# Optimization experiments

Measured on AMD Instinct MI355X. Metric: run time of the kernel, lower is better.

The kernel has to match this reference:

```python
import jax, jax.numpy as jnp
import numpy as np

DT = 0.5  # timestep; CFL-stable for c<1, grid spacing h=1


def laplace5(u):
    # 5-point Laplacian with zero (Dirichlet) boundary, grid spacing 1.
    # u: [B, Nx, Ny]
    z = jnp.pad(u, ((0, 0), (1, 1), (1, 1)))
    return (z[:, 2:, 1:-1] + z[:, :-2, 1:-1]
            + z[:, 1:-1, 2:] + z[:, 1:-1, :-2] - 4.0 * u)


def setup_inputs() -> dict:
    key = jax.random.key(0)
    k1, k2, k3, k4, k5 = jax.random.split(key, 5)
    B, T, Nx, Ny, Np = 16, 256, 256, 256, 3
    x = jax.random.normal(k1, (B, T), dtype=jnp.float32)
    c = jax.random.uniform(k2, (Nx, Ny), dtype=jnp.float32)      # wave speed
    b = jax.random.uniform(k3, (Nx, Ny), dtype=jnp.float32)      # damping (rho)
    px = jax.random.randint(k4, (Np,), 0, Nx)
    py = jax.random.randint(k5, (Np,), 0, Ny)
    return {"x": x, "c": c, "b": b, "px": px, "py": py, "sx": 128, "sy": 128}


def reference(x, c, b, px, py, sx, sy):
    # x: [B, T], c,b: [Nx, Ny]; returns y: [B, T, Np]
    B = x.shape[0]
    Nx, Ny = c.shape
    c1 = 1.0 / (1.0 + 0.5 * DT * b)          # [Nx, Ny]
    c2 = 1.0 - 0.5 * DT * b                  # [Nx, Ny]
    csq_dt2 = (DT * DT) * (c * c)            # [Nx, Ny]
    h0 = jnp.zeros((B, Nx, Ny), dtype=x.dtype)

    def step(carry, xi):
        h1, h2 = carry
        # wave cell: second-order leapfrog with damping
        hn = c1 * (2.0 * h1 - c2 * h2 + csq_dt2 * laplace5(h1))
        # point source injection of scalar input per batch element
        hn = hn.at[:, sx, sy].add(xi)
        # point probes -> [B, Np]
        y = hn[:, px, py]
        return (hn, h1), y

    xt = jnp.transpose(x, (1, 0))            # [T, B]
    _, ys = jax.lax.scan(step, (h0, h0), xt)  # ys: [T, B, Np]
    return jnp.transpose(ys, (1, 0, 2))       # [B, T, Np]
```

## Files before the change

### kernel.cpp

```cpp
#include <hip/hip_runtime.h>


#define B_    16
#define T_    256
#define NY    256
#define NP    3
#define NSLAB 8
#define WAVES 8
#define THREADS 512
#define NIF   (NSLAB - 1)
#define KCH   4
#define NCHUNK (T_ / KCH)

__device__ uint64_t g_halo[B_][NIF][2][2][8][NY];

__global__ void reset_halo()
{
    const int n = B_ * NIF * 2 * 2 * 8 * NY;
    int i = blockIdx.x * blockDim.x + threadIdx.x;
    if (i < n) (&g_halo[0][0][0][0][0][0])[i] = 0ull;
}

#define PACK(tag, f) (((uint64_t)(uint32_t)(tag) << 32) | (uint64_t)__float_as_uint(f))

#define SUB(H1, H2, GA, GB, K_, TT) do { \
    __syncthreads(); \
    const int p_ = (K_) & 1; \
    const int q_ = ((K_) + 1) & 1; \
    float up_[4], dn_[4]; \
    if (w == 0) { \
        if (s == 0) { _Pragma("unroll") for (int j = 0; j < 4; ++j) up_[j] = 0.f; } \
        else        { _Pragma("unroll") for (int j = 0; j < 4; ++j) up_[j] = GA[3][j]; } \
    } else { \
        const float4 u4_ = *reinterpret_cast<const float4*>(&botL[p_][w - 1][y0]); \
        up_[0] = u4_.x; up_[1] = u4_.y; up_[2] = u4_.z; up_[3] = u4_.w; \
    } \
    if (w == WAVES - 1) { \
        if (s == NSLAB - 1) { _Pragma("unroll") for (int j = 0; j < 4; ++j) dn_[j] = 0.f; } \
        else                { _Pragma("unroll") for (int j = 0; j < 4; ++j) dn_[j] = GA[0][j]; } \
    } else { \
        const float4 d4_ = *reinterpret_cast<const float4*>(&topL[p_][w + 1][y0]); \
        dn_[0] = d4_.x; dn_[1] = d4_.y; dn_[2] = d4_.z; dn_[3] = d4_.w; \
    } \
     \
    _Pragma("unroll") for (int r = 0; r < 4; ++r) { \
        float lf_ = __shfl_up(H1[r][3], 1, 64); \
        float rt_ = __shfl_down(H1[r][0], 1, 64); \
        if (l == 0)  lf_ = 0.f; \
        if (l == 63) rt_ = 0.f; \
        _Pragma("unroll") for (int j = 0; j < 4; ++j) { \
            const float lv_ = (j == 0) ? lf_ : H1[r][j - 1]; \
            const float rv_ = (j == 3) ? rt_ : H1[r][j + 1]; \
            const float av_ = (r == 0) ? up_[j] : H1[r - 1][j]; \
            const float dv_ = (r == 3) ? dn_[j] : H1[r + 1][j]; \
            const float s4_ = (av_ + dv_) + (lv_ + rv_); \
            const float d_  = H1[r][j] - H2[r][j]; \
            const float e_  = fmaf(-4.0f, H1[r][j], s4_); \
            float v_ = fmaf(CC[r][j], e_, H2[r][j]); \
            v_ = fmaf(TC[r][j], d_, v_); \
            H2[r][j] = v_; \
        } \
    } \
     \
    if (upG) { \
        _Pragma("unroll") for (int i = 1; i < 4; ++i) { \
            if (i >= (K_) + 1) { \
                float lf_ = __shfl_up(GA[i][3], 1, 64); \
                float rt_ = __shfl_down(GA[i][0], 1, 64); \
                if (l == 0)  lf_ = 0.f; \
                if (l == 63) rt_ = 0.f; \
                _Pragma("unroll") for (int j = 0; j < 4; ++j) { \
                    const float lv_ = (j == 0) ? lf_ : GA[i][j - 1]; \
                    const float rv_ = (j == 3) ? rt_ : GA[i][j + 1]; \
                    const float av_ = GA[i - 1][j]; \
                    const float dv_ = (i == 3) ? H1[0][j] : GA[i + 1][j]; \
                    const float s4_ = (av_ + dv_) + (lv_ + rv_); \
                    const float d_  = GA[i][j] - GB[i][j]; \
                    const float e_  = fmaf(-4.0f, GA[i][j], s4_); \
                    float v_ = fmaf(gCC[i][j], e_, GB[i][j]); \
                    v_ = fmaf(gTC[i][j], d_, v_); \
                    if (gsrcHere && i == gsrc_r && j == gsrc_c) v_ += xbuf[TT]; \
                    GB[i][j] = v_; \
                } \
            } \
        } \
    } \
    if (dnG) { \
        _Pragma("unroll") for (int i = 0; i < 3; ++i) { \
            if (i <= 2 - (K_)) { \
                float lf_ = __shfl_up(GA[i][3], 1, 64); \
                float rt_ = __shfl_down(GA[i][0], 1, 64); \
                if (l == 0)  lf_ = 0.f; \
                if (l == 63) rt_ = 0.f; \
                _Pragma("unroll") for (int j = 0; j < 4; ++j) { \
                    const float lv_ = (j == 0) ? lf_ : GA[i][j - 1]; \
                    const float rv_ = (j == 3) ? rt_ : GA[i][j + 1]; \
                    const float av_ = (i == 0) ? H1[3][j] : GA[i - 1][j]; \
                    const float dv_ = GA[i + 1][j]; \
                    const float s4_ = (av_ + dv_) + (lv_ + rv_); \
                    const float d_  = GA[i][j] - GB[i][j]; \
                    const float e_  = fmaf(-4.0f, GA[i][j], s4_); \
                    float v_ = fmaf(gCC[i][j], e_, GB[i][j]); \
                    v_ = fmaf(gTC[i][j], d_, v_); \
                    if (gsrcHere && i == gsrc_r && j == gsrc_c) v_ += xbuf[TT]; \
                    GB[i][j] = v_; \
                } \
            } \
        } \
    } \
     \
    if (srcHere) { \
        const float xv_ = xbuf[TT]; \
        _Pragma("unroll") for (int r = 0; r < 4; ++r) \
            _Pragma("unroll") for (int j = 0; j < 4; ++j) \
                if (r == src_r && j == src_c) H2[r][j] += xv_; \
    } \
     \
    _Pragma("unroll") for (int qq = 0; qq < NP; ++qq) { \
        if (pHere[qq]) { \
            float v_ = 0.f; \
            _Pragma("unroll") for (int r = 0; r < 4; ++r) \
                _Pragma("unroll") for (int j = 0; j < 4; ++j) \
                    if (r == pr[qq] && j == pc[qq]) v_ = H2[r][j]; \
            out[((size_t)b * T_ + (TT)) * NP + qq] = v_; \
        } \
    } \
     \
    *reinterpret_cast<float4*>(&topL[q_][w][y0]) = make_float4(H2[0][0], H2[0][1], H2[0][2], H2[0][3]); \
    *reinterpret_cast<float4*>(&botL[q_][w][y0]) = make_float4(H2[3][0], H2[3][1], H2[3][2], H2[3][3]); \
} while (0)

__launch_bounds__(THREADS, 1)
__global__ void wave_multi(const float* __restrict__ xin,
                           const float* __restrict__ cin,
                           const float* __restrict__ bin,
                           const int* __restrict__ pxp,
                           const int* __restrict__ pyp,
                           const int* __restrict__ sxp,
                           const int* __restrict__ syp,
                           float* __restrict__ out)
{
    const int blk = blockIdx.x;
    const int b = blk >> 3;
    const int s = blk & 7;
    const int tid = threadIdx.x;
    const int w = tid >> 6;
    const int l = tid & 63;
    const int r0 = s * 32 + w * 4;
    const int y0 = l * 4;

    __shared__ float xbuf[T_];
    __shared__ float topL[2][WAVES][NY];
    __shared__ float botL[2][WAVES][NY];

    for (int i = tid; i < WAVES * NY; i += THREADS) {
        (&topL[0][0][0])[i] = 0.f;
        (&botL[0][0][0])[i] = 0.f;
    }
    if (tid < T_) xbuf[tid] = xin[b * T_ + tid];

    float h1[4][4], h2[4][4], TC[4][4], CC[4][4];
#pragma unroll
    for (int r = 0; r < 4; ++r) {
        const float4 cv = *reinterpret_cast<const float4*>(&cin[(r0 + r) * NY + y0]);
        const float4 bv = *reinterpret_cast<const float4*>(&bin[(r0 + r) * NY + y0]);
        const float cvv[4] = {cv.x, cv.y, cv.z, cv.w};
        const float bvv[4] = {bv.x, bv.y, bv.z, bv.w};
#pragma unroll
        for (int j = 0; j < 4; ++j) {
            const float c1  = 1.0f / (1.0f + 0.25f * bvv[j]);
            const float csq = 0.25f * cvv[j] * cvv[j];
            TC[r][j] = 2.0f * c1;
            CC[r][j] = c1 * csq;
            h1[r][j] = 0.f;
            h2[r][j] = 0.f;
        }
    }

    const bool upG = (w == 0 && s > 0);
    const bool dnG = (w == WAVES - 1 && s < NSLAB - 1);
    const int gr0 = upG ? (r0 - 4) : (dnG ? (r0 + 4) : r0);
    float ga[4][4], gb[4][4], gTC[4][4], gCC[4][4];
#pragma unroll
    for (int i = 0; i < 4; ++i) {
        const float4 cv = *reinterpret_cast<const float4*>(&cin[(gr0 + i) * NY + y0]);
        const float4 bv = *reinterpret_cast<const float4*>(&bin[(gr0 + i) * NY + y0]);
        const float cvv[4] = {cv.x, cv.y, cv.z, cv.w};
        const float bvv[4] = {bv.x, bv.y, bv.z, bv.w};
#pragma unroll
        for (int j = 0; j < 4; ++j) {
            const float c1  = 1.0f / (1.0f + 0.25f * bvv[j]);
            const float csq = 0.25f * cvv[j] * cvv[j];
            gTC[i][j] = 2.0f * c1;
            gCC[i][j] = c1 * csq;
            ga[i][j] = 0.f;
            gb[i][j] = 0.f;
        }
    }

    const int sx = sxp[0], sy = syp[0];
    const bool srcHere = (sx >= r0 && sx < r0 + 4 && sy >= y0 && sy < y0 + 4);
    const int  src_r = sx - r0, src_c = sy - y0;
    const bool gsrcHere = (upG || dnG) && (sx >= gr0 && sx < gr0 + 4 && sy >= y0 && sy < y0 + 4);
    const int  gsrc_r = sx - gr0, gsrc_c = sy - y0;
    bool pHere[NP];
    int  pr[NP], pc[NP];
#pragma unroll
    for (int q = 0; q < NP; ++q) {
        const int pxx = pxp[q], pyy = pyp[q];
        pHere[q] = (pxx >= r0 && pxx < r0 + 4 && pyy >= y0 && pyy < y0 + 4);
        pr[q] = pxx - r0;
        pc[q] = pyy - y0;
    }

#pragma unroll 1
    for (int c = 0; c < NCHUNK; ++c) {
        if ((c > 0) && (upG || dnG)) {
            const int iface = upG ? (s - 1) : s;
            const int side  = upG ? 0 : 1;
            uint64_t* gp = &g_halo[b][iface][side][c & 1][0][0];
            uint64_t vv[8][4];
            bool ok;
            do {
                ok = true;
#pragma unroll
                for (int rf = 0; rf < 8; ++rf)
#pragma unroll
                    for (int j = 0; j < 4; ++j)
                        vv[rf][j] = __hip_atomic_load(gp + rf * NY + j * 64 + l,
                                                      __ATOMIC_RELAXED, __HIP_MEMORY_SCOPE_AGENT);
#pragma unroll
                for (int rf = 0; rf < 8; ++rf)
#pragma unroll
                    for (int j = 0; j < 4; ++j)
                        ok = ok && ((uint32_t)(vv[rf][j] >> 32) == (uint32_t)c);
            } while (!ok);
#pragma unroll
            for (int i = 0; i < 4; ++i)
#pragma unroll
                for (int j = 0; j < 4; ++j) {
                    ga[i][j] = __uint_as_float((uint32_t)vv[i][j]);
                    gb[i][j] = __uint_as_float((uint32_t)vv[4 + i][j]);
                }
        }

        SUB(h1, h2, ga, gb, 0, 4 * c + 0);
        SUB(h2, h1, gb, ga, 1, 4 * c + 1);
        SUB(h1, h2, ga, gb, 2, 4 * c + 2);
        SUB(h2, h1, gb, ga, 3, 4 * c + 3);

        if ((c + 1 < NCHUNK) && (upG || dnG)) {
            const int iface = upG ? (s - 1) : s;
            const int side  = upG ? 1 : 0;
            uint64_t* gp = &g_halo[b][iface][side][(c + 1) & 1][0][0];
#pragma unroll
            for (int i = 0; i < 4; ++i)
#pragma unroll
                for (int j = 0; j < 4; ++j) {
                    __hip_atomic_store(gp + i * NY + j * 64 + l, PACK(c + 1, h1[i][j]),
                                       __ATOMIC_RELAXED, __HIP_MEMORY_SCOPE_AGENT);
                    __hip_atomic_store(gp + (4 + i) * NY + j * 64 + l, PACK(c + 1, h2[i][j]),
                                       __ATOMIC_RELAXED, __HIP_MEMORY_SCOPE_AGENT);
                }
        }
    }
}

extern "C" void kernel_launch(void* const* d_in, const int* in_sizes, int n_in,
                              void* d_out, int out_size, void* d_ws, size_t ws_size,
                              hipStream_t stream)
{
    const float* x  = (const float*)d_in[0];
    const float* c  = (const float*)d_in[1];
    const float* bb = (const float*)d_in[2];
    const int*   px = (const int*)d_in[3];
    const int*   py = (const int*)d_in[4];
    const int*   sx = (const int*)d_in[5];
    const int*   sy = (const int*)d_in[6];
    float* out = (float*)d_out;

    const int words = B_ * NIF * 2 * 2 * 8 * NY;
    reset_halo<<<(words + 255) / 256, 256, 0, stream>>>();

    void* args[] = { (void*)&x, (void*)&c, (void*)&bb, (void*)&px, (void*)&py,
                     (void*)&sx, (void*)&sy, (void*)&out };
    hipLaunchCooperativeKernel(reinterpret_cast<void*>(wave_multi),
                               dim3(B_ * NSLAB), dim3(THREADS), args, 0, stream);
}
```

Before: 428.0 us.

## Replace per-step block barrier with per-wave LDS flag handshakes and overlap interior rows

```diff
diff --git a/kernel.cpp b/kernel.cpp
--- a/kernel.cpp
+++ b/kernel.cpp
@@ -23,45 +23,39 @@
 
 #define PACK(tag, f) (((uint64_t)(uint32_t)(tag) << 32) | (uint64_t)__float_as_uint(f))
 
-#define SUB(H1, H2, GA, GB, K_, TT) do { \
-    __syncthreads(); \
-    const int p_ = (K_) & 1; \
-    const int q_ = ((K_) + 1) & 1; \
-    float up_[4], dn_[4]; \
-    if (w == 0) { \
-        if (s == 0) { _Pragma("unroll") for (int j = 0; j < 4; ++j) up_[j] = 0.f; } \
-        else        { _Pragma("unroll") for (int j = 0; j < 4; ++j) up_[j] = GA[3][j]; } \
-    } else { \
-        const float4 u4_ = *reinterpret_cast<const float4*>(&botL[p_][w - 1][y0]); \
-        up_[0] = u4_.x; up_[1] = u4_.y; up_[2] = u4_.z; up_[3] = u4_.w; \
-    } \
-    if (w == WAVES - 1) { \
-        if (s == NSLAB - 1) { _Pragma("unroll") for (int j = 0; j < 4; ++j) dn_[j] = 0.f; } \
-        else                { _Pragma("unroll") for (int j = 0; j < 4; ++j) dn_[j] = GA[0][j]; } \
-    } else { \
-        const float4 d4_ = *reinterpret_cast<const float4*>(&topL[p_][w + 1][y0]); \
-        dn_[0] = d4_.x; dn_[1] = d4_.y; dn_[2] = d4_.z; dn_[3] = d4_.w; \
-    } \
-     \
-    _Pragma("unroll") for (int r = 0; r < 4; ++r) { \
-        float lf_ = __shfl_up(H1[r][3], 1, 64); \
-        float rt_ = __shfl_down(H1[r][0], 1, 64); \
-        if (l == 0)  lf_ = 0.f; \
-        if (l == 63) rt_ = 0.f; \
-        _Pragma("unroll") for (int j = 0; j < 4; ++j) { \
-            const float lv_ = (j == 0) ? lf_ : H1[r][j - 1]; \
-            const float rv_ = (j == 3) ? rt_ : H1[r][j + 1]; \
-            const float av_ = (r == 0) ? up_[j] : H1[r - 1][j]; \
-            const float dv_ = (r == 3) ? dn_[j] : H1[r + 1][j]; \
-            const float s4_ = (av_ + dv_) + (lv_ + rv_); \
-            const float d_  = H1[r][j] - H2[r][j]; \
-            const float e_  = fmaf(-4.0f, H1[r][j], s4_); \
-            float v_ = fmaf(CC[r][j], e_, H2[r][j]); \
-            v_ = fmaf(TC[r][j], d_, v_); \
-            H2[r][j] = v_; \
+#define ROWC(H1, H2, r, UPA, DNA) do { \
+    float lf_ = __shfl_up(H1[r][3], 1, 64); \
+    float rt_ = __shfl_down(H1[r][0], 1, 64); \
+    if (l == 0)  lf_ = 0.f; \
+    if (l == 63) rt_ = 0.f; \
+    _Pragma("unroll") for (int j = 0; j < 4; ++j) { \
+        const float lv_ = (j == 0) ? lf_ : H1[r][j - 1]; \
+        const float rv_ = (j == 3) ? rt_ : H1[r][j + 1]; \
+        const float s4_ = (UPA[j] + DNA[j]) + (lv_ + rv_); \
+        const float d_  = H1[r][j] - H2[r][j]; \
+        const float e_  = fmaf(-4.0f, H1[r][j], s4_); \
+        float v_ = fmaf(CC[r][j], e_, H2[r][j]); \
+        v_ = fmaf(TC[r][j], d_, v_); \
+        H2[r][j] = v_; \
+    } \
+} while (0)
+
+#define SRCP(H2, r, TT) do { \
+    if (srcHere && src_r == (r)) { \
+        _Pragma("unroll") for (int j = 0; j < 4; ++j) \
+            if (src_c == j) H2[r][j] += xbuf[TT]; \
+    } \
+    _Pragma("unroll") for (int qq = 0; qq < NP; ++qq) { \
+        if (pHere[qq] && pr[qq] == (r)) { \
+            float v_ = 0.f; \
+            _Pragma("unroll") for (int j = 0; j < 4; ++j) \
+                if (pc[qq] == j) v_ = H2[r][j]; \
+            out[((size_t)b * T_ + (TT)) * NP + qq] = v_; \
         } \
     } \
-     \
+} while (0)
+
+#define GHOSTS(H1, GA, GB, K_, TT) do { \
     if (upG) { \
         _Pragma("unroll") for (int i = 1; i < 4; ++i) { \
             if (i >= (K_) + 1) { \
@@ -108,29 +102,53 @@
             } \
         } \
     } \
-     \
-    if (srcHere) { \
-        const float xv_ = xbuf[TT]; \
-        _Pragma("unroll") for (int r = 0; r < 4; ++r) \
-            _Pragma("unroll") for (int j = 0; j < 4; ++j) \
-                if (r == src_r && j == src_c) H2[r][j] += xv_; \
-    } \
-     \
-    _Pragma("unroll") for (int qq = 0; qq < NP; ++qq) { \
-        if (pHere[qq]) { \
-            float v_ = 0.f; \
-            _Pragma("unroll") for (int r = 0; r < 4; ++r) \
-                _Pragma("unroll") for (int j = 0; j < 4; ++j) \
-                    if (r == pr[qq] && j == pc[qq]) v_ = H2[r][j]; \
-            out[((size_t)b * T_ + (TT)) * NP + qq] = v_; \
-        } \
-    } \
-     \
-    *reinterpret_cast<float4*>(&topL[q_][w][y0]) = make_float4(H2[0][0], H2[0][1], H2[0][2], H2[0][3]); \
-    *reinterpret_cast<float4*>(&botL[q_][w][y0]) = make_float4(H2[3][0], H2[3][1], H2[3][2], H2[3][3]); \
 } while (0)
 
-__launch_bounds__(THREADS, 1)
+#define SUB(H1, H2, GA, GB, K_, TT) do { \
+    const int P_ = (K_) & 1; \
+    const int Q_ = ((K_) + 1) & 1; \
+    ROWC(H1, H2, 1, H1[0], H1[2]); \
+    ROWC(H1, H2, 2, H1[1], H1[3]); \
+    float gu_[4], gd_[4]; \
+    if (w == 0) { \
+        if (s == 0) { gu_[0] = gu_[1] = gu_[2] = gu_[3] = 0.f; } \
+        else { gu_[0] = GA[3][0]; gu_[1] = GA[3][1]; gu_[2] = GA[3][2]; gu_[3] = GA[3][3]; } \
+    } else { \
+        while (__hip_atomic_load(&r3t[w - 1][P_], __ATOMIC_RELAXED, __HIP_MEMORY_SCOPE_WORKGROUP) != (TT)) {} \
+        asm volatile("" ::: "memory"); \
+        const float4 u4_ = *reinterpret_cast<const float4*>(&r3v[w - 1][P_][y0]); \
+        gu_[0] = u4_.x; gu_[1] = u4_.y; gu_[2] = u4_.z; gu_[3] = u4_.w; \
+    } \
+    if (w == WAVES - 1) { \
+        if (s == NSLAB - 1) { gd_[0] = gd_[1] = gd_[2] = gd_[3] = 0.f; } \
+        else { gd_[0] = GA[0][0]; gd_[1] = GA[0][1]; gd_[2] = GA[0][2]; gd_[3] = GA[0][3]; } \
+    } else { \
+        while (__hip_atomic_load(&r0t[w + 1][P_], __ATOMIC_RELAXED, __HIP_MEMORY_SCOPE_WORKGROUP) != (TT)) {} \
+        asm volatile("" ::: "memory"); \
+        const float4 d4_ = *reinterpret_cast<const float4*>(&r0v[w + 1][P_][y0]); \
+        gd_[0] = d4_.x; gd_[1] = d4_.y; gd_[2] = d4_.z; gd_[3] = d4_.w; \
+    } \
+    ROWC(H1, H2, 0, gu_, H1[1]); \
+    ROWC(H1, H2, 3, H1[2], gd_); \
+    SRCP(H2, 0, TT); \
+    SRCP(H2, 3, TT); \
+    if (w > 0) \
+        *reinterpret_cast<float4*>(&r0v[w][Q_][y0]) = make_float4(H2[0][0], H2[0][1], H2[0][2], H2[0][3]); \
+    if (w < WAVES - 1) \
+        *reinterpret_cast<float4*>(&r3v[w][Q_][y0]) = make_float4(H2[3][0], H2[3][1], H2[3][2], H2[3][3]); \
+    asm volatile("s_waitcnt lgkmcnt(0)" ::: "memory"); \
+    if (l == 0) { \
+        if (w > 0) \
+            __hip_atomic_store(&r0t[w][Q_], (TT) + 1, __ATOMIC_RELAXED, __HIP_MEMORY_SCOPE_WORKGROUP); \
+        if (w < WAVES - 1) \
+            __hip_atomic_store(&r3t[w][Q_], (TT) + 1, __ATOMIC_RELAXED, __HIP_MEMORY_SCOPE_WORKGROUP); \
+    } \
+    GHOSTS(H1, GA, GB, K_, TT); \
+    SRCP(H2, 1, TT); \
+    SRCP(H2, 2, TT); \
+} while (0)
+
+__launch_bounds__(THREADS, 2)
 __global__ void wave_multi(const float* __restrict__ xin,
                            const float* __restrict__ cin,
                            const float* __restrict__ bin,
@@ -150,12 +168,19 @@
     const int y0 = l * 4;
 
     __shared__ float xbuf[T_];
-    __shared__ float topL[2][WAVES][NY];
-    __shared__ float botL[2][WAVES][NY];
-
-    for (int i = tid; i < WAVES * NY; i += THREADS) {
-        (&topL[0][0][0])[i] = 0.f;
-        (&botL[0][0][0])[i] = 0.f;
+    __shared__ float r0v[WAVES][2][NY];
+    __shared__ float r3v[WAVES][2][NY];
+    __shared__ int   r0t[WAVES][2];
+    __shared__ int   r3t[WAVES][2];
+
+    for (int i = tid; i < WAVES * 2 * NY; i += THREADS) {
+        (&r0v[0][0][0])[i] = 0.f;
+        (&r3v[0][0][0])[i] = 0.f;
+    }
+    if (tid < WAVES * 2) {
+        const int w_ = tid >> 1, p_ = tid & 1;
+        r0t[w_][p_] = (p_ == 0) ? 0 : -1;
+        r3t[w_][p_] = (p_ == 0) ? 0 : -1;
     }
     if (tid < T_) xbuf[tid] = xin[b * T_ + tid];
 
@@ -212,6 +237,8 @@
         pr[q] = pxx - r0;
         pc[q] = pyy - y0;
     }
+
+    __syncthreads();
 
 #pragma unroll 1
     for (int c = 0; c < NCHUNK; ++c) {
```

Result: slower. 439.9 us (+2.8%).
